# Kernel optimization log

Hardware: AMD Instinct MI355X
Metric: run time of the kernel (lower is better)

Reference implementation:

```python
import jax, jax.numpy as jnp
import numpy as np

NH = 4        # n_head
L_TOPK = 16   # AWG top-k l
DEC = 2       # dec_layers
EPS = 1e-6


def _ln(x, g, b):
    m = jnp.mean(x, -1, keepdims=True)
    v = jnp.mean((x - m) ** 2, -1, keepdims=True)
    return (x - m) * jax.lax.rsqrt(v + EPS) * g + b


def _heads(x, W):
    B, L, C = x.shape
    return (x @ W).reshape(B, L, NH, C // NH).transpose(0, 2, 1, 3)  # [B,H,L,dk]


def _softmax_attn(qh, kh):
    dk = qh.shape[-1]
    logits = jnp.einsum('bhqd,bhkd->bhqk', qh / jnp.sqrt(jnp.float32(dk)), kh)
    return jax.nn.softmax(logits, axis=-1)


def cross_attn_block(q, k, v, Wq, Wk, Wv, Wo, g, b):
    B, Lq, C = q.shape
    a = _softmax_attn(_heads(q, Wq), _heads(k, Wk))
    o = jnp.einsum('bhqk,bhkd->bhqd', a, _heads(v, Wv))
    o = o.transpose(0, 2, 1, 3).reshape(B, Lq, C) @ Wo
    return _ln(o + q, g, b)


def awg_attn_block(q, k, v, Wq, Wk, Wv, Wo, g, b):
    # top-k attention-weight-gating: keep weights >= l-th largest, renormalize
    B, Lq, C = q.shape
    a = _softmax_attn(_heads(q, Wq), _heads(k, Wk))
    thr = jax.lax.top_k(a, L_TOPK)[0][..., -1:]          # [B,H,Lq,1]
    w = a * (a >= thr).astype(a.dtype)
    w = w / jnp.sum(w, -1, keepdims=True)
    o = jnp.einsum('bhqk,bhkd->bhqd', w, _heads(v, Wv))
    o = o.transpose(0, 2, 1, 3).reshape(B, Lq, C) @ Wo
    return _ln(o + q, g, b)


def setup_inputs() -> dict:
    key = jax.random.key(0)
    ks = jax.random.split(key, 32)
    B, Lq, Lk, C, F = 4, 3000, 750, 64, 256
    s = 1.0 / np.sqrt(C)
    sf = 1.0 / np.sqrt(F)
    d = {}
    d['q'] = jax.random.normal(ks[0], (B, Lq, C), jnp.float32)
    d['enc'] = jax.random.normal(ks[1], (B, Lk, C), jnp.float32)
    # cross_attn_layer params
    for i, n in enumerate(['cal_Wq', 'cal_Wk', 'cal_Wv', 'cal_Wo']):
        d[n] = jax.random.normal(ks[2 + i], (C, C), jnp.float32) * s
    d['cal_ln1_g'] = jnp.ones((C,), jnp.float32)
    d['cal_ln1_b'] = jnp.zeros((C,), jnp.float32)
    d['cal_W1'] = jax.random.normal(ks[6], (C, F), jnp.float32) * s
    d['cal_b1'] = jnp.zeros((F,), jnp.float32)
    d['cal_W2'] = jax.random.normal(ks[7], (F, C), jnp.float32) * sf
    d['cal_b2'] = jnp.zeros((C,), jnp.float32)
    d['cal_ln2_g'] = jnp.ones((C,), jnp.float32)
    d['cal_ln2_b'] = jnp.zeros((C,), jnp.float32)
    # stacked MGAN params [DEC, ...]
    d['m_ln_g'] = jnp.ones((DEC, C), jnp.float32)
    d['m_ln_b'] = jnp.zeros((DEC, C), jnp.float32)
    d['m_fc1_W'] = jax.random.normal(ks[8], (DEC, C, C), jnp.float32) * s
    d['m_fc1_b'] = jnp.zeros((DEC, C), jnp.float32)
    d['m_fc2_W'] = jax.random.normal(ks[9], (DEC, C, C), jnp.float32) * s
    d['m_fc2_b'] = jnp.zeros((DEC, C), jnp.float32)
    for i, n in enumerate(['m_Wq', 'm_Wk', 'm_Wv', 'm_Wo']):
        d[n] = jax.random.normal(ks[10 + i], (DEC, C, C), jnp.float32) * s
    d['m_aln_g'] = jnp.ones((DEC, C), jnp.float32)
    d['m_aln_b'] = jnp.zeros((DEC, C), jnp.float32)
    d['fc_W'] = jax.random.normal(ks[14], (C, 1), jnp.float32) * s
    d['fc_b'] = jnp.zeros((1,), jnp.float32)
    return d


def reference(q, enc, cal_Wq, cal_Wk, cal_Wv, cal_Wo, cal_ln1_g, cal_ln1_b,
              cal_W1, cal_b1, cal_W2, cal_b2, cal_ln2_g, cal_ln2_b,
              m_ln_g, m_ln_b, m_fc1_W, m_fc1_b, m_fc2_W, m_fc2_b,
              m_Wq, m_Wk, m_Wv, m_Wo, m_aln_g, m_aln_b, fc_W, fc_b):
    # cross_attn_layer: attention + FFN + LN (dropout = identity in eval)
    x = cross_attn_block(q, enc, enc, cal_Wq, cal_Wk, cal_Wv, cal_Wo, cal_ln1_g, cal_ln1_b)
    ffn = jax.nn.relu(x @ cal_W1 + cal_b1) @ cal_W2 + cal_b2
    x = _ln(ffn + x, cal_ln2_g, cal_ln2_b)
    # MGAN decoder layers (rep_KV: k,v = encoder output)
    for i in range(DEC):
        qn = _ln(x, m_ln_g[i], m_ln_b[i])
        sg = jax.nn.sigmoid(qn @ m_fc1_W[i] + m_fc1_b[i]) * (qn @ m_fc2_W[i] + m_fc2_b[i])
        awg = awg_attn_block(sg, enc, enc, m_Wq[i], m_Wk[i], m_Wv[i], m_Wo[i],
                             m_aln_g[i], m_aln_b[i])
        # GLU(cat(sg, awg)) = sg * sigmoid(awg)
        x = qn + sg * jax.nn.sigmoid(awg)
    # label_type='p' head
    return jax.nn.sigmoid(x @ fc_W + fc_b)  # [B, Lq, 1]
```

## Files before the change

### kernel.cpp

```cpp
#include <hip/hip_runtime.h>
#include <hip/hip_bf16.h>

using bf16 = __hip_bfloat16;

#define DEV_INLINE __device__ __forceinline__

constexpr int B_  = 4;
constexpr int LQ  = 3000;
constexpr int LK  = 750;
constexpr int NH_ = 4;
constexpr float EPSF = 1e-6f;

constexpr int PITCH = 751;

constexpr size_t WS_KV = 0;
constexpr size_t WS_XB = 1152000;
constexpr size_t WS_QP = 1920000;
constexpr size_t WS_AO = 2688000;
constexpr size_t WS_QN = 3456000;
constexpr size_t WS_SG = 4224000;

typedef _Float16 half2_t __attribute__((ext_vector_type(2)));
typedef _Float16 half4_t __attribute__((ext_vector_type(4)));
typedef float    f32x4   __attribute__((ext_vector_type(4)));

#define MFMA16(a, b, c) __builtin_amdgcn_mfma_f32_16x16x16f16((a), (b), (c), 0, 0, 0)

DEV_INLINE float sigmoidf(float x) { return 1.f / (1.f + __expf(-x)); }

DEV_INLINE unsigned int packh2(float a, float b) {
  half2_t h = { (_Float16)a, (_Float16)b };
  unsigned int u; __builtin_memcpy(&u, &h, 4); return u;
}
DEV_INLINE half2_t u2h(unsigned int u) {
  half2_t h; __builtin_memcpy(&h, &u, 4); return h;
}
DEV_INLINE unsigned short f2h(float f) {
  _Float16 h = (_Float16)f;
  unsigned short u; __builtin_memcpy(&u, &h, 2); return u;
}
DEV_INLINE half4_t h4_from(const unsigned short* p) {
  unsigned int lo = *(const unsigned int*)p;
  unsigned int hi = *(const unsigned int*)(p + 2);
  unsigned long long v = ((unsigned long long)hi << 32) | lo;
  half4_t h; __builtin_memcpy(&h, &v, 8); return h;
}
DEV_INLINE float dot2(unsigned int kw, half2_t qh, float acc) {
  return __builtin_amdgcn_fdot2(u2h(kw), qh, acc, false);
}

DEV_INLINE unsigned int f2sort(float f) {
  int ib = __float_as_int(f);
  return (unsigned int)(ib ^ ((ib >> 31) | 0x80000000));
}
DEV_INLINE float sort2f(unsigned int u) {
  const int ib = (u & 0x80000000u) ? (int)(u ^ 0x80000000u) : (int)~u;
  return __int_as_float(ib);
}

DEV_INLINE unsigned int bcastu(unsigned int v) {
  return (unsigned int)__builtin_amdgcn_readfirstlane((int)v);
}

DEV_INLINE void sort64u_desc4(unsigned int v[4]) {
  const int lane = threadIdx.x & 63;
  #pragma unroll
  for (int k = 2; k <= 64; k <<= 1) {
    #pragma unroll
    for (int j = k >> 1; j > 0; j >>= 1) {
      const bool takeMax = ((lane & j) == 0) == ((lane & k) == 0);
      #pragma unroll
      for (int r = 0; r < 4; ++r) {
        const unsigned int o = __shfl_xor(v[r], j);
        v[r] = (takeMax == (v[r] > o)) ? v[r] : o;
      }
    }
  }
}

DEV_INLINE float row_ln(float v, float g, float b) {
  float s1 = v, s2 = v * v;
  #pragma unroll
  for (int off = 32; off > 0; off >>= 1) {
    s1 += __shfl_xor(s1, off);
    s2 += __shfl_xor(s2, off);
  }
  const float m   = s1 * (1.f / 64.f);
  const float var = s2 * (1.f / 64.f) - m * m;
  return (v - m) * rsqrtf(var + EPSF) * g + b;
}

__global__ __launch_bounds__(256) void kvq_proj_kernel(
    const float* __restrict__ enc, const float* __restrict__ q,
    const float* __restrict__ calWq,
    const float* __restrict__ calWk, const float* __restrict__ calWv,
    const float* __restrict__ mWk, const float* __restrict__ mWv,
    float* __restrict__ kv, float* __restrict__ qp)
{
  const int y = blockIdx.y;
  if (y < 6 && blockIdx.x >= 188) return;
  __shared__ float Wl[64 * 65];
  __shared__ float xs[16][64];
  const int t = threadIdx.x, rr = t >> 6, cc = t & 63;
  const float* W;
  const float* src;
  float* dst;
  float scale = 1.f;
  int nrows = 3000;
  switch (y) {
    case 0: W = calWk; src = enc; dst = kv;               break;
    case 1: W = calWv; src = enc; dst = kv + 192000;      break;
    case 2: W = mWk;        src = enc; dst = kv + 384000; break;
    case 3: W = mWv;        src = enc; dst = kv + 576000; break;
    case 4: W = mWk + 4096; src = enc; dst = kv + 768000; break;
    case 5: W = mWv + 4096; src = enc; dst = kv + 960000; break;
    default: W = calWq; src = q; dst = qp; scale = 0.25f; nrows = 12000; break;
  }
  const bool packK = (y == 2) || (y == 4);
  for (int i = t; i < 4096; i += 256) Wl[(i >> 6) * 65 + (i & 63)] = W[i];
  const int base = blockIdx.x * 16;
  for (int i = t; i < 1024; i += 256) {
    const int grow = base + (i >> 6);
    xs[i >> 6][i & 63] = (grow < nrows) ? src[(size_t)grow * 64 + (i & 63)] : 0.f;
  }
  __syncthreads();
  #pragma unroll
  for (int p = 0; p < 4; ++p) {
    const int row = p * 4 + rr;
    const int grow = base + row;
    float acc = 0.f;
    #pragma unroll
    for (int c = 0; c < 64; ++c) acc = fmaf(xs[row][c], Wl[c * 65 + cc], acc);
    if (packK) {
      const float accN = __shfl_xor(acc, 1);
      if (!(cc & 1) && grow < nrows)
        ((unsigned int*)dst)[(size_t)grow * 32 + (cc >> 1)] = packh2(acc, accN);
    } else if (grow < nrows) {
      dst[(size_t)grow * 64 + cc] = acc * scale;
    }
  }
}

__global__ __launch_bounds__(256) void cross_attn_kernel(
    const float* __restrict__ qp, const float* __restrict__ kp,
    const float* __restrict__ vp, float* __restrict__ ao)
{
  extern __shared__ char smem[];
  unsigned short* Kl = (unsigned short*)smem;
  unsigned short* Vt = Kl + 750 * 18;
  unsigned short* Pt = Vt + 16 * 754;

  const int t = threadIdx.x;
  const int h = blockIdx.y, b = blockIdx.z;
  const float* kslab = kp + (size_t)(b * LK) * 64 + h * 16;
  const float* vslab = vp + (size_t)(b * LK) * 64 + h * 16;

  for (int k = t; k < LK; k += 256) {
    const float4* ks = (const float4*)(kslab + (size_t)k * 64);
    const float4* vs = (const float4*)(vslab + (size_t)k * 64);
    unsigned int* kr = (unsigned int*)(Kl + k * 18);
    #pragma unroll
    for (int q4 = 0; q4 < 4; ++q4) {
      float4 a = ks[q4], v = vs[q4];
      kr[q4 * 2]     = packh2(a.x, a.y);
      kr[q4 * 2 + 1] = packh2(a.z, a.w);
      Vt[(q4 * 4 + 0) * 754 + k] = f2h(v.x);
      Vt[(q4 * 4 + 1) * 754 + k] = f2h(v.y);
      Vt[(q4 * 4 + 2) * 754 + k] = f2h(v.z);
      Vt[(q4 * 4 + 3) * 754 + k] = f2h(v.w);
    }
  }
  if (t < 32) Vt[(t & 15) * 754 + 750 + (t >> 4)] = 0;
  __syncthreads();

  const int wave = t >> 6, lane = t & 63;
  const int col = lane & 15, quad = lane >> 4;
  const int qbase = blockIdx.x * 64 + wave * 16;
  unsigned short* Pt_w = Pt + wave * 288;

  int qrow = qbase + col; if (qrow >= LQ) qrow = LQ - 1;
  const float* qptr = qp + ((size_t)(b * LQ + qrow)) * 64 + h * 16 + quad * 4;
  half4_t aQ;
  {
    unsigned long long v = ((unsigned long long)packh2(qptr[2], qptr[3]) << 32)
                         | packh2(qptr[0], qptr[1]);
    __builtin_memcpy(&aQ, &v, 8);
  }

  f32x4 O = {0.f, 0.f, 0.f, 0.f};
  float Zp[4] = {0.f, 0.f, 0.f, 0.f};
  const f32x4 zeroC = {0.f, 0.f, 0.f, 0.f};

  for (int tile = 0; tile < 47; ++tile) {
    const int key = tile * 16 + col;
    const half4_t bK = h4_from(Kl + key * 18 + quad * 4);
    f32x4 S = MFMA16(aQ, bK, zeroC);
    const bool valid = key < LK;
    float e0 = valid ? __expf(S[0]) : 0.f;
    float e1 = valid ? __expf(S[1]) : 0.f;
    float e2 = valid ? __expf(S[2]) : 0.f;
    float e3 = valid ? __expf(S[3]) : 0.f;
    Zp[0] += e0; Zp[1] += e1; Zp[2] += e2; Zp[3] += e3;
    Pt_w[(quad * 4 + 0) * 18 + col] = f2h(e0);
    Pt_w[(quad * 4 + 1) * 18 + col] = f2h(e1);
    Pt_w[(quad * 4 + 2) * 18 + col] = f2h(e2);
    Pt_w[(quad * 4 + 3) * 18 + col] = f2h(e3);
    const half4_t aP = h4_from(Pt_w + col * 18 + quad * 4);
    const half4_t bV = h4_from(Vt + col * 754 + tile * 16 + quad * 4);
    O = MFMA16(aP, bV, O);
  }

  #pragma unroll
  for (int r = 0; r < 4; ++r) {
    float z = Zp[r];
    z += __shfl_xor(z, 1);
    z += __shfl_xor(z, 2);
    z += __shfl_xor(z, 4);
    z += __shfl_xor(z, 8);
    Zp[r] = z;
  }

  #pragma unroll
  for (int r = 0; r < 4; ++r) {
    const int orow = qbase + quad * 4 + r;
    if (orow < LQ)
      ao[((size_t)(b * LQ + orow)) * 64 + h * 16 + col] = O[r] / Zp[r];
  }
}

__global__ __launch_bounds__(512) void awg_attn_kernel(
    const float* __restrict__ qp, const unsigned int* __restrict__ kp,
    const float* __restrict__ vp, float* __restrict__ ao)
{
  extern __shared__ char smem[];
  uint2*          KT2   = (uint2*)smem;
  unsigned int*   candV = (unsigned int*)(smem + 4 * PITCH * 8);
  unsigned short* candK = (unsigned short*)(smem + 4 * PITCH * 8 + 8192);
  float*          selW  = (float*)(smem + 4 * PITCH * 8 + 8192 + 4096);
  unsigned short* selK  = (unsigned short*)(smem + 4 * PITCH * 8 + 8192 + 4096 + 3072);

  const int t = threadIdx.x;
  const int h = blockIdx.y, b = blockIdx.z;
  const unsigned int* kslab = kp + ((size_t)(b * LK)) * 32 + h * 8;

  for (int k = t; k < LK; k += 512) {
    const uint2* ks = (const uint2*)(kslab + (size_t)k * 32);
    #pragma unroll
    for (int d4 = 0; d4 < 4; ++d4) KT2[d4 * PITCH + k] = ks[d4];
  }
  __syncthreads();

  const int wave = t >> 6, lane = t & 63;
  const unsigned long long below = (1ull << lane) - 1ull;
  unsigned int*   cV = candV + wave * 256;
  unsigned short* cK = candK + wave * 256;
  float*          sW = selW + wave * 96;
  unsigned short* sK = selK + wave * 96;

  sW[lane] = -3.0e38f; sK[lane] = 0;
  if (lane < 32) { sW[64 + lane] = -3.0e38f; sK[64 + lane] = 0; }
  #pragma unroll
  for (int r = 0; r < 4; ++r) cV[r * 64 + lane] = 0u;

  const int r0 = blockIdx.x * 32 + wave * 4;
  int r0r = r0; if (r0r > LQ - 4) r0r = LQ - 4;
  const float* qrow = qp + ((size_t)(b * LQ + r0r)) * 64 + h * 16;
  unsigned int qw[4][8];
  #pragma unroll
  for (int r = 0; r < 4; ++r) {
    #pragma unroll
    for (int i = 0; i < 8; ++i)
      qw[r][i] = bcastu(packh2(qrow[r * 64 + 2 * i], qrow[r * 64 + 2 * i + 1]));
  }

  float lg[4][12];
  #pragma unroll
  for (int tt = 0; tt < 12; ++tt) {
    const int k = lane + (tt << 6);
    if (tt < 11 || k < LK) {
      float a0 = 0.f, a1 = 0.f, a2 = 0.f, a3 = 0.f;
      #pragma unroll
      for (int d4 = 0; d4 < 4; ++d4) {
        const uint2 w = KT2[d4 * PITCH + k];
        a0 = dot2(w.x, u2h(qw[0][2 * d4]), a0); a0 = dot2(w.y, u2h(qw[0][2 * d4 + 1]), a0);
        a1 = dot2(w.x, u2h(qw[1][2 * d4]), a1); a1 = dot2(w.y, u2h(qw[1][2 * d4 + 1]), a1);
        a2 = dot2(w.x, u2h(qw[2][2 * d4]), a2); a2 = dot2(w.y, u2h(qw[2][2 * d4 + 1]), a2);
        a3 = dot2(w.x, u2h(qw[3][2 * d4]), a3); a3 = dot2(w.y, u2h(qw[3][2 * d4 + 1]), a3);
      }
      lg[0][tt] = a0; lg[1][tt] = a1; lg[2][tt] = a2; lg[3][tt] = a3;
    } else {
      lg[0][tt] = -3.0e38f; lg[1][tt] = -3.0e38f;
      lg[2][tt] = -3.0e38f; lg[3][tt] = -3.0e38f;
    }
  }

  unsigned int hs[4];
  #pragma unroll
  for (int r = 0; r < 4; ++r) {
    float m = lg[r][0];
    #pragma unroll
    for (int tt = 1; tt < 12; ++tt) m = fmaxf(m, lg[r][tt]);
    hs[r] = f2sort(m);
  }

  sort64u_desc4(hs);
  unsigned int L[4];
  #pragma unroll
  for (int r = 0; r < 4; ++r) L[r] = __shfl(hs[r], 15);

  int cb[4] = {0, 0, 0, 0};
  #pragma unroll
  for (int tt = 0; tt < 12; ++tt) {
    const int k = lane + (tt << 6);
    #pragma unroll
    for (int r = 0; r < 4; ++r) {
      const unsigned int s = f2sort(lg[r][tt]);
      const bool p = s >= L[r];
      const unsigned long long m = __ballot(p);
      if (p) {
        const int pos = cb[r] + (int)__popcll(m & below);
        if (pos < 64) { cV[r * 64 + pos] = s; cK[r * 64 + pos] = (unsigned short)k; }
      }
      cb[r] += (int)__popcll(m);
    }
  }

  unsigned int su[4], so[4];
  #pragma unroll
  for (int r = 0; r < 4; ++r) { su[r] = cV[r * 64 + lane]; so[r] = su[r]; }
  sort64u_desc4(so);
  unsigned int T[4]; float Mv[4];
  #pragma unroll
  for (int r = 0; r < 4; ++r) {
    T[r]  = __shfl(so[r], 15);
    Mv[r] = sort2f(__shfl(so[r], 0));
  }

  #pragma unroll
  for (int r = 0; r < 4; ++r) {
    const bool w = su[r] >= T[r];
    const unsigned long long mw = __ballot(w);
    if (w) {
      const int pos = (int)__popcll(mw & below);
      if (pos < 24) { sW[r * 24 + pos] = sort2f(su[r]); sK[r * 24 + pos] = cK[r * 64 + lane]; }
    }
  }

  const int dd = lane & 15;
  const int rsel = lane >> 4;
  const float ref = (rsel == 0) ? Mv[0] : (rsel == 1) ? Mv[1] : (rsel == 2) ? Mv[2] : Mv[3];
  const float* cwr = sW + rsel * 24;
  const unsigned short* cir = sK + rsel * 24;
  const float* vbase = vp + (size_t)(b * LK) * 64 + h * 16 + dd;
  float acc = 0.f, Z = 0.f;
  #pragma unroll
  for (int j = 0; j < 24; ++j) {
    const float e = __expf(cwr[j] - ref);
    Z += e;
    acc = fmaf(e, vbase[(size_t)cir[j] * 64], acc);
  }
  if (r0 + rsel < LQ)
    ao[((size_t)(b * LQ + r0 + rsel)) * 64 + h * 16 + dd] = acc / Z;
}

__global__ __launch_bounds__(256) void ffn_pre_kernel(
    const float* __restrict__ ao, const float* __restrict__ qres,
    const float* __restrict__ Wo,
    const float* __restrict__ g1, const float* __restrict__ b1n,
    const float* __restrict__ W1, const float* __restrict__ bb1,
    const float* __restrict__ W2, const float* __restrict__ bb2,
    const float* __restrict__ g2, const float* __restrict__ b2n,
    const float* __restrict__ lng, const float* __restrict__ lnb,
    const float* __restrict__ fc1W, const float* __restrict__ fc1b,
    const float* __restrict__ fc2W, const float* __restrict__ fc2b,
    const float* __restrict__ Wq,
    float* __restrict__ qn, float* __restrict__ sg, float* __restrict__ qp)
{
  __shared__ float xs[16][64];
  __shared__ float hsm[16][256];
  const int t = threadIdx.x, rr = t >> 6, cc = t & 63;
  const size_t base = (size_t)blockIdx.x * 16;
  for (int i = t; i < 1024; i += 256) xs[i >> 6][i & 63] = ao[base * 64 + i];
  __syncthreads();
  float acc[4];
  #pragma unroll
  for (int p = 0; p < 4; ++p) acc[p] = 0.f;
  #pragma unroll 8
  for (int c = 0; c < 64; ++c) {
    const float w = Wo[c * 64 + cc];
    #pragma unroll
    for (int p = 0; p < 4; ++p) acc[p] = fmaf(xs[p * 4 + rr][c], w, acc[p]);
  }
  #pragma unroll
  for (int p = 0; p < 4; ++p) acc[p] += qres[(base + p * 4 + rr) * 64 + cc];
  __syncthreads();
  float x1[4];
  #pragma unroll
  for (int p = 0; p < 4; ++p) {
    x1[p] = row_ln(acc[p], g1[cc], b1n[cc]);
    xs[p * 4 + rr][cc] = x1[p];
  }
  __syncthreads();
  {
    float hv[16];
    #pragma unroll
    for (int r = 0; r < 16; ++r) hv[r] = 0.f;
    #pragma unroll 4
    for (int c = 0; c < 64; ++c) {
      const float w = W1[c * 256 + t];
      #pragma unroll
      for (int r = 0; r < 16; ++r) hv[r] = fmaf(xs[r][c], w, hv[r]);
    }
    const float bb = bb1[t];
    #pragma unroll
    for (int r = 0; r < 16; ++r) hsm[r][t] = fmaxf(hv[r] + bb, 0.f);
  }
  __syncthreads();
  float acc2[4];
  #pragma unroll
  for (int p = 0; p < 4; ++p) acc2[p] = bb2[cc];
  #pragma unroll 8
  for (int c = 0; c < 256; ++c) {
    const float w = W2[c * 64 + cc];
    #pragma unroll
    for (int p = 0; p < 4; ++p) acc2[p] = fmaf(hsm[p * 4 + rr][c], w, acc2[p]);
  }
  float qv[4];
  #pragma unroll
  for (int p = 0; p < 4; ++p) {
    const float xv = row_ln(acc2[p] + x1[p], g2[cc], b2n[cc]);
    qv[p] = row_ln(xv, lng[cc], lnb[cc]);
    qn[(base + p * 4 + rr) * 64 + cc] = qv[p];
  }
  __syncthreads();
  #pragma unroll
  for (int p = 0; p < 4; ++p) xs[p * 4 + rr][cc] = qv[p];
  __syncthreads();
  float d1[4], d2[4];
  #pragma unroll
  for (int p = 0; p < 4; ++p) { d1[p] = fc1b[cc]; d2[p] = fc2b[cc]; }
  #pragma unroll 4
  for (int c = 0; c < 64; ++c) {
    const float w1 = fc1W[c * 64 + cc];
    const float w2 = fc2W[c * 64 + cc];
    #pragma unroll
    for (int p = 0; p < 4; ++p) {
      const float xq = xs[p * 4 + rr][c];
      d1[p] = fmaf(xq, w1, d1[p]);
      d2[p] = fmaf(xq, w2, d2[p]);
    }
  }
  float sv[4];
  #pragma unroll
  for (int p = 0; p < 4; ++p) {
    sv[p] = sigmoidf(d1[p]) * d2[p];
    sg[(base + p * 4 + rr) * 64 + cc] = sv[p];
  }
  __syncthreads();
  #pragma unroll
  for (int p = 0; p < 4; ++p) xs[p * 4 + rr][cc] = sv[p];
  __syncthreads();
  float aq[4];
  #pragma unroll
  for (int p = 0; p < 4; ++p) aq[p] = 0.f;
  #pragma unroll 8
  for (int c = 0; c < 64; ++c) {
    const float w = Wq[c * 64 + cc];
    #pragma unroll
    for (int p = 0; p < 4; ++p) aq[p] = fmaf(xs[p * 4 + rr][c], w, aq[p]);
  }
  #pragma unroll
  for (int p = 0; p < 4; ++p)
    qp[(base + p * 4 + rr) * 64 + cc] = aq[p] * 0.25f;
}

__global__ __launch_bounds__(256) void out_pre_kernel(
    const float* __restrict__ ao, const float* __restrict__ sg,
    const float* __restrict__ qn, const float* __restrict__ Wo,
    const float* __restrict__ g_, const float* __restrict__ b_,
    const float* __restrict__ lng, const float* __restrict__ lnb,
    const float* __restrict__ W1, const float* __restrict__ bb1,
    const float* __restrict__ W2, const float* __restrict__ bb2,
    const float* __restrict__ Wq,
    float* __restrict__ qn_out, float* __restrict__ sg_out,
    float* __restrict__ qp_out)
{
  __shared__ float xs[16][64];
  const int t = threadIdx.x, rr = t >> 6, cc = t & 63;
  const size_t base = (size_t)blockIdx.x * 16;
  for (int i = t; i < 1024; i += 256) xs[i >> 6][i & 63] = ao[base * 64 + i];
  __syncthreads();
  float accp[4], sgv[4];
  #pragma unroll
  for (int p = 0; p < 4; ++p) accp[p] = 0.f;
  #pragma unroll 8
  for (int c = 0; c < 64; ++c) {
    const float w = Wo[c * 64 + cc];
    #pragma unroll
    for (int p = 0; p < 4; ++p) accp[p] = fmaf(xs[p * 4 + rr][c], w, accp[p]);
  }
  #pragma unroll
  for (int p = 0; p < 4; ++p) {
    sgv[p] = sg[(base + p * 4 + rr) * 64 + cc];
    accp[p] += sgv[p];
  }
  __syncthreads();
  float qv[4];
  #pragma unroll
  for (int p = 0; p < 4; ++p) {
    const size_t idx = (base + p * 4 + rr) * 64 + cc;
    const float awg = row_ln(accp[p], g_[cc], b_[cc]);
    const float xv = qn[idx] + sgv[p] * sigmoidf(awg);
    qv[p] = row_ln(xv, lng[cc], lnb[cc]);
    qn_out[idx] = qv[p];
    xs[p * 4 + rr][cc] = qv[p];
  }
  __syncthreads();
  float d1[4], d2[4];
  #pragma unroll
  for (int p = 0; p < 4; ++p) { d1[p] = bb1[cc]; d2[p] = bb2[cc]; }
  #pragma unroll 4
  for (int c = 0; c < 64; ++c) {
    const float w1 = W1[c * 64 + cc];
    const float w2 = W2[c * 64 + cc];
    #pragma unroll
    for (int p = 0; p < 4; ++p) {
      const float xv = xs[p * 4 + rr][c];
      d1[p] = fmaf(xv, w1, d1[p]);
      d2[p] = fmaf(xv, w2, d2[p]);
    }
  }
  __syncthreads();
  float sv[4];
  #pragma unroll
  for (int p = 0; p < 4; ++p) {
    sv[p] = sigmoidf(d1[p]) * d2[p];
    sg_out[(base + p * 4 + rr) * 64 + cc] = sv[p];
    xs[p * 4 + rr][cc] = sv[p];
  }
  __syncthreads();
  float aq[4];
  #pragma unroll
  for (int p = 0; p < 4; ++p) aq[p] = 0.f;
  #pragma unroll 8
  for (int c = 0; c < 64; ++c) {
    const float w = Wq[c * 64 + cc];
    #pragma unroll
    for (int p = 0; p < 4; ++p) aq[p] = fmaf(xs[p * 4 + rr][c], w, aq[p]);
  }
  #pragma unroll
  for (int p = 0; p < 4; ++p)
    qp_out[(base + p * 4 + rr) * 64 + cc] = aq[p] * 0.25f;
}

__global__ __launch_bounds__(256) void out_final_kernel(
    const float* __restrict__ ao, const float* __restrict__ sg,
    const float* __restrict__ qn, const float* __restrict__ Wo,
    const float* __restrict__ g_, const float* __restrict__ b_,
    const float* __restrict__ fw, const float* __restrict__ fb,
    float* __restrict__ out)
{
  __shared__ float xs[16][64];
  const int t = threadIdx.x, rr = t >> 6, cc = t & 63;
  const size_t base = (size_t)blockIdx.x * 16;
  for (int i = t; i < 1024; i += 256) xs[i >> 6][i & 63] = ao[base * 64 + i];
  __syncthreads();
  float accp[4];
  #pragma unroll
  for (int p = 0; p < 4; ++p) accp[p] = 0.f;
  #pragma unroll 8
  for (int c = 0; c < 64; ++c) {
    const float w = Wo[c * 64 + cc];
    #pragma unroll
    for (int p = 0; p < 4; ++p) accp[p] = fmaf(xs[p * 4 + rr][c], w, accp[p]);
  }
  #pragma unroll
  for (int p = 0; p < 4; ++p) {
    const size_t idx = (base + p * 4 + rr) * 64 + cc;
    const float sgv = sg[idx];
    const float a = accp[p] + sgv;
    const float awg = row_ln(a, g_[cc], b_[cc]);
    const float xv = qn[idx] + sgv * sigmoidf(awg);
    float v = xv * fw[cc];
    #pragma unroll
    for (int off = 32; off > 0; off >>= 1) v += __shfl_xor(v, off);
    if (cc == 0) out[base + p * 4 + rr] = sigmoidf(v + fb[0]);
  }
}

extern "C" void kernel_launch(void* const* d_in, const int* in_sizes, int n_in,
                              void* d_out, int out_size, void* d_ws, size_t ws_size,
                              hipStream_t stream) {
  (void)in_sizes; (void)n_in; (void)out_size; (void)ws_size;

  const float* q     = (const float*)d_in[0];
  const float* enc   = (const float*)d_in[1];
  const float* calWq = (const float*)d_in[2];
  const float* calWk = (const float*)d_in[3];
  const float* calWv = (const float*)d_in[4];
  const float* calWo = (const float*)d_in[5];
  const float* ln1g  = (const float*)d_in[6];
  const float* ln1b  = (const float*)d_in[7];
  const float* W1    = (const float*)d_in[8];
  const float* b1v   = (const float*)d_in[9];
  const float* W2    = (const float*)d_in[10];
  const float* b2v   = (const float*)d_in[11];
  const float* ln2g  = (const float*)d_in[12];
  const float* ln2b  = (const float*)d_in[13];
  const float* mlng  = (const float*)d_in[14];
  const float* mlnb  = (const float*)d_in[15];
  const float* mfc1W = (const float*)d_in[16];
  const float* mfc1b = (const float*)d_in[17];
  const float* mfc2W = (const float*)d_in[18];
  const float* mfc2b = (const float*)d_in[19];
  const float* mWq   = (const float*)d_in[20];
  const float* mWk   = (const float*)d_in[21];
  const float* mWv   = (const float*)d_in[22];
  const float* mWo   = (const float*)d_in[23];
  const float* malng = (const float*)d_in[24];
  const float* malnb = (const float*)d_in[25];
  const float* fcW   = (const float*)d_in[26];
  const float* fcb   = (const float*)d_in[27];
  float* out = (float*)d_out;

  float* ws  = (float*)d_ws;
  float* kv  = ws + WS_KV;
  float* qp  = ws + WS_QP;
  float* aob = ws + WS_AO;
  float* qnb = ws + WS_QN;
  float* sgb = ws + WS_SG;

  const size_t crossLds = (750 * 18 + 16 * 754 + 4 * 288) * 2;
  const size_t awgLds   = 4 * PITCH * 8 + 8192 + 4096 + 3072 + 1536;

  kvq_proj_kernel<<<dim3(750, 7), 256, 0, stream>>>(enc, q, calWq, calWk, calWv,
                                                    mWk, mWv, kv, qp);

  cross_attn_kernel<<<dim3(47, NH_, B_), 256, crossLds, stream>>>(qp, kv, kv + 192000, aob);
  ffn_pre_kernel<<<750, 256, 0, stream>>>(aob, q, calWo, ln1g, ln1b,
                                          W1, b1v, W2, b2v, ln2g, ln2b,
                                          mlng, mlnb, mfc1W, mfc1b,
                                          mfc2W, mfc2b, mWq, qnb, sgb, qp);

  awg_attn_kernel<<<dim3(94, NH_, B_), 512, awgLds, stream>>>(
      qp, (const unsigned int*)(kv + 2 * 192000), kv + 3 * 192000, aob);
  out_pre_kernel<<<750, 256, 0, stream>>>(aob, sgb, qnb, mWo, malng, malnb,
                                          mlng + 64, mlnb + 64,
                                          mfc1W + 4096, mfc1b + 64,
                                          mfc2W + 4096, mfc2b + 64,
                                          mWq + 4096, qnb, sgb, qp);

  awg_attn_kernel<<<dim3(94, NH_, B_), 512, awgLds, stream>>>(
      qp, (const unsigned int*)(kv + 4 * 192000), kv + 5 * 192000, aob);
  out_final_kernel<<<750, 256, 0, stream>>>(aob, sgb, qnb, mWo + 4096,
                                            malng + 64, malnb + 64, fcW, fcb, out);
}
```

Baseline: 319.3 us.

## Compute AWG logits with MFMA into shared memory; read projection weights directly

Result: slower. 326.4 us (+2.2%).

```diff
diff --git a/kernel.cpp b/kernel.cpp
--- a/kernel.cpp
+++ b/kernel.cpp
@@ -11,7 +11,7 @@
 constexpr int NH_ = 4;
 constexpr float EPSF = 1e-6f;
 
-constexpr int PITCH = 751;
+constexpr int LGP = 758;
 
 constexpr size_t WS_KV = 0;
 constexpr size_t WS_XB = 1152000;
@@ -45,9 +45,6 @@
   unsigned long long v = ((unsigned long long)hi << 32) | lo;
   half4_t h; __builtin_memcpy(&h, &v, 8); return h;
 }
-DEV_INLINE float dot2(unsigned int kw, half2_t qh, float acc) {
-  return __builtin_amdgcn_fdot2(u2h(kw), qh, acc, false);
-}
 
 DEV_INLINE unsigned int f2sort(float f) {
   int ib = __float_as_int(f);
@@ -56,10 +53,6 @@
 DEV_INLINE float sort2f(unsigned int u) {
   const int ib = (u & 0x80000000u) ? (int)(u ^ 0x80000000u) : (int)~u;
   return __int_as_float(ib);
-}
-
-DEV_INLINE unsigned int bcastu(unsigned int v) {
-  return (unsigned int)__builtin_amdgcn_readfirstlane((int)v);
 }
 
 DEV_INLINE void sort64u_desc4(unsigned int v[4]) {
@@ -99,7 +92,6 @@
 {
   const int y = blockIdx.y;
   if (y < 6 && blockIdx.x >= 188) return;
-  __shared__ float Wl[64 * 65];
   __shared__ float xs[16][64];
   const int t = threadIdx.x, rr = t >> 6, cc = t & 63;
   const float* W;
@@ -117,26 +109,28 @@
     default: W = calWq; src = q; dst = qp; scale = 0.25f; nrows = 12000; break;
   }
   const bool packK = (y == 2) || (y == 4);
-  for (int i = t; i < 4096; i += 256) Wl[(i >> 6) * 65 + (i & 63)] = W[i];
   const int base = blockIdx.x * 16;
   for (int i = t; i < 1024; i += 256) {
     const int grow = base + (i >> 6);
     xs[i >> 6][i & 63] = (grow < nrows) ? src[(size_t)grow * 64 + (i & 63)] : 0.f;
   }
   __syncthreads();
-  #pragma unroll
-  for (int p = 0; p < 4; ++p) {
-    const int row = p * 4 + rr;
-    const int grow = base + row;
-    float acc = 0.f;
-    #pragma unroll
-    for (int c = 0; c < 64; ++c) acc = fmaf(xs[row][c], Wl[c * 65 + cc], acc);
+  float acc[4] = {0.f, 0.f, 0.f, 0.f};
+  #pragma unroll 8
+  for (int c = 0; c < 64; ++c) {
+    const float w = W[c * 64 + cc];
+    #pragma unroll
+    for (int p = 0; p < 4; ++p) acc[p] = fmaf(xs[p * 4 + rr][c], w, acc[p]);
+  }
+  #pragma unroll
+  for (int p = 0; p < 4; ++p) {
+    const int grow = base + p * 4 + rr;
     if (packK) {
-      const float accN = __shfl_xor(acc, 1);
+      const float accN = __shfl_xor(acc[p], 1);
       if (!(cc & 1) && grow < nrows)
-        ((unsigned int*)dst)[(size_t)grow * 32 + (cc >> 1)] = packh2(acc, accN);
+        ((unsigned int*)dst)[(size_t)grow * 32 + (cc >> 1)] = packh2(acc[p], accN);
     } else if (grow < nrows) {
-      dst[(size_t)grow * 64 + cc] = acc * scale;
+      dst[(size_t)grow * 64 + cc] = acc[p] * scale;
     }
   }
 }
@@ -228,29 +222,57 @@
   }
 }
 
-__global__ __launch_bounds__(512) void awg_attn_kernel(
+__global__ __launch_bounds__(256) void awg_attn_kernel(
     const float* __restrict__ qp, const unsigned int* __restrict__ kp,
     const float* __restrict__ vp, float* __restrict__ ao)
 {
   extern __shared__ char smem[];
-  uint2*          KT2   = (uint2*)smem;
-  unsigned int*   candV = (unsigned int*)(smem + 4 * PITCH * 8);
-  unsigned short* candK = (unsigned short*)(smem + 4 * PITCH * 8 + 8192);
-  float*          selW  = (float*)(smem + 4 * PITCH * 8 + 8192 + 4096);
-  unsigned short* selK  = (unsigned short*)(smem + 4 * PITCH * 8 + 8192 + 4096 + 3072);
+  float* Lg = (float*)smem;
+  unsigned int*   candV = (unsigned int*)smem;
+  unsigned short* candK = (unsigned short*)(smem + 4096);
+  float*          selW  = (float*)(smem + 4096 + 2048);
+  unsigned short* selK  = (unsigned short*)(smem + 4096 + 2048 + 1536);
 
   const int t = threadIdx.x;
   const int h = blockIdx.y, b = blockIdx.z;
-  const unsigned int* kslab = kp + ((size_t)(b * LK)) * 32 + h * 8;
-
-  for (int k = t; k < LK; k += 512) {
-    const uint2* ks = (const uint2*)(kslab + (size_t)k * 32);
-    #pragma unroll
-    for (int d4 = 0; d4 < 4; ++d4) KT2[d4 * PITCH + k] = ks[d4];
-  }
-  __syncthreads();
-
   const int wave = t >> 6, lane = t & 63;
+  const int col = lane & 15, quad = lane >> 4;
+  const int rbase = blockIdx.x * 16;
+
+  int qrow = rbase + col; if (qrow >= LQ) qrow = LQ - 1;
+  const float* qptr = qp + ((size_t)(b * LQ + qrow)) * 64 + h * 16 + quad * 4;
+  half4_t aQ;
+  {
+    unsigned long long v = ((unsigned long long)packh2(qptr[2], qptr[3]) << 32)
+                         | packh2(qptr[0], qptr[1]);
+    __builtin_memcpy(&aQ, &v, 8);
+  }
+  const unsigned int* kslab = kp + ((size_t)(b * LK)) * 32 + h * 8 + quad * 2;
+  const f32x4 zeroC = {0.f, 0.f, 0.f, 0.f};
+  for (int tile = wave; tile < 47; tile += 4) {
+    const int key = tile * 16 + col;
+    const int keyc = (key < LK) ? key : LK - 1;
+    const uint2 w = *(const uint2*)(kslab + (size_t)keyc * 32);
+    unsigned long long v = ((unsigned long long)w.y << 32) | w.x;
+    half4_t bK; __builtin_memcpy(&bK, &v, 8);
+    f32x4 S = MFMA16(aQ, bK, zeroC);
+    const bool valid = key < LK;
+    #pragma unroll
+    for (int r = 0; r < 4; ++r)
+      Lg[(quad * 4 + r) * LGP + key] = valid ? S[r] : -3.0e38f;
+  }
+  __syncthreads();
+
+  float lg[4][12];
+  #pragma unroll
+  for (int tt = 0; tt < 12; ++tt) {
+    const int k = lane + (tt << 6);
+    #pragma unroll
+    for (int r = 0; r < 4; ++r)
+      lg[r][tt] = (tt < 11 || k < LK) ? Lg[(wave * 4 + r) * LGP + k] : -3.0e38f;
+  }
+  __syncthreads();
+
   const unsigned long long below = (1ull << lane) - 1ull;
   unsigned int*   cV = candV + wave * 256;
   unsigned short* cK = candK + wave * 256;
@@ -262,51 +284,21 @@
   #pragma unroll
   for (int r = 0; r < 4; ++r) cV[r * 64 + lane] = 0u;
 
-  const int r0 = blockIdx.x * 32 + wave * 4;
-  int r0r = r0; if (r0r > LQ - 4) r0r = LQ - 4;
-  const float* qrow = qp + ((size_t)(b * LQ + r0r)) * 64 + h * 16;
-  unsigned int qw[4][8];
-  #pragma unroll
-  for (int r = 0; r < 4; ++r) {
-    #pragma unroll
-    for (int i = 0; i < 8; ++i)
-      qw[r][i] = bcastu(packh2(qrow[r * 64 + 2 * i], qrow[r * 64 + 2 * i + 1]));
-  }
-
-  float lg[4][12];
-  #pragma unroll
-  for (int tt = 0; tt < 12; ++tt) {
-    const int k = lane + (tt << 6);
-    if (tt < 11 || k < LK) {
-      float a0 = 0.f, a1 = 0.f, a2 = 0.f, a3 = 0.f;
-      #pragma unroll
-      for (int d4 = 0; d4 < 4; ++d4) {
-        const uint2 w = KT2[d4 * PITCH + k];
-        a0 = dot2(w.x, u2h(qw[0][2 * d4]), a0); a0 = dot2(w.y, u2h(qw[0][2 * d4 + 1]), a0);
-        a1 = dot2(w.x, u2h(qw[1][2 * d4]), a1); a1 = dot2(w.y, u2h(qw[1][2 * d4 + 1]), a1);
-        a2 = dot2(w.x, u2h(qw[2][2 * d4]), a2); a2 = dot2(w.y, u2h(qw[2][2 * d4 + 1]), a2);
-        a3 = dot2(w.x, u2h(qw[3][2 * d4]), a3); a3 = dot2(w.y, u2h(qw[3][2 * d4 + 1]), a3);
-      }
-      lg[0][tt] = a0; lg[1][tt] = a1; lg[2][tt] = a2; lg[3][tt] = a3;
-    } else {
-      lg[0][tt] = -3.0e38f; lg[1][tt] = -3.0e38f;
-      lg[2][tt] = -3.0e38f; lg[3][tt] = -3.0e38f;
-    }
-  }
-
-  unsigned int hs[4];
+  const int r0 = rbase + wave * 4;
+
+  unsigned int hs4[4];
   #pragma unroll
   for (int r = 0; r < 4; ++r) {
     float m = lg[r][0];
     #pragma unroll
     for (int tt = 1; tt < 12; ++tt) m = fmaxf(m, lg[r][tt]);
-    hs[r] = f2sort(m);
-  }
-
-  sort64u_desc4(hs);
+    hs4[r] = f2sort(m);
+  }
+
+  sort64u_desc4(hs4);
   unsigned int L[4];
   #pragma unroll
-  for (int r = 0; r < 4; ++r) L[r] = __shfl(hs[r], 15);
+  for (int r = 0; r < 4; ++r) L[r] = __shfl(hs4[r], 15);
 
   int cb[4] = {0, 0, 0, 0};
   #pragma unroll
@@ -631,7 +623,7 @@
   float* sgb = ws + WS_SG;
 
   const size_t crossLds = (750 * 18 + 16 * 754 + 4 * 288) * 2;
-  const size_t awgLds   = 4 * PITCH * 8 + 8192 + 4096 + 3072 + 1536;
+  const size_t awgLds   = 16 * LGP * 4;
 
   kvq_proj_kernel<<<dim3(750, 7), 256, 0, stream>>>(enc, q, calWq, calWk, calWv,
                                                     mWk, mWv, kv, qp);
@@ -642,7 +634,7 @@
                                           mlng, mlnb, mfc1W, mfc1b,
                                           mfc2W, mfc2b, mWq, qnb, sgb, qp);
 
-  awg_attn_kernel<<<dim3(94, NH_, B_), 512, awgLds, stream>>>(
+  awg_attn_kernel<<<dim3(188, NH_, B_), 256, awgLds, stream>>>(
       qp, (const unsigned int*)(kv + 2 * 192000), kv + 3 * 192000, aob);
   out_pre_kernel<<<750, 256, 0, stream>>>(aob, sgb, qnb, mWo, malng, malnb,
                                           mlng + 64, mlnb + 64,
@@ -650,7 +642,7 @@
                                           mfc2W + 4096, mfc2b + 64,
                                           mWq + 4096, qnb, sgb, qp);
 
-  awg_attn_kernel<<<dim3(94, NH_, B_), 512, awgLds, stream>>>(
+  awg_attn_kernel<<<dim3(188, NH_, B_), 256, awgLds, stream>>>(
       qp, (const unsigned int*)(kv + 4 * 192000), kv + 5 * 192000, aob);
   out_final_kernel<<<750, 256, 0, stream>>>(aob, sgb, qnb, mWo + 4096,
                                             malng + 64, malnb + 64, fcW, fcb, out);
```

## Pre-transpose weight matrices and use float4 vectorized GEMV loads

Applied to the files above, without the earlier changes.

Result: slower. 376.9 us (+18.1%).

```diff
diff --git a/kernel.cpp b/kernel.cpp
--- a/kernel.cpp
+++ b/kernel.cpp
@@ -90,53 +90,122 @@
   return (v - m) * rsqrtf(var + EPSF) * g + b;
 }
 
+__global__ __launch_bounds__(256) void transpose_kernel(
+    const float* __restrict__ calWq, const float* __restrict__ calWk,
+    const float* __restrict__ calWv, const float* __restrict__ calWo,
+    const float* __restrict__ mWk, const float* __restrict__ mWv,
+    const float* __restrict__ mWq, const float* __restrict__ mWo,
+    const float* __restrict__ fc1, const float* __restrict__ fc2,
+    const float* __restrict__ W1, const float* __restrict__ W2,
+    float* __restrict__ dst)
+{
+  const int b = blockIdx.x, t = threadIdx.x;
+  if (b < 16) {
+    const float* src;
+    switch (b) {
+      case 0:  src = calWq;        break;
+      case 1:  src = calWk;        break;
+      case 2:  src = calWv;        break;
+      case 3:  src = calWo;        break;
+      case 4:  src = mWk;          break;
+      case 5:  src = mWk + 4096;   break;
+      case 6:  src = mWv;          break;
+      case 7:  src = mWv + 4096;   break;
+      case 8:  src = mWq;          break;
+      case 9:  src = mWq + 4096;   break;
+      case 10: src = mWo;          break;
+      case 11: src = mWo + 4096;   break;
+      case 12: src = fc1;          break;
+      case 13: src = fc1 + 4096;   break;
+      case 14: src = fc2;          break;
+      default: src = fc2 + 4096;   break;
+    }
+    float* d = dst + b * 4096;
+    for (int i = t; i < 4096; i += 256) {
+      const int r = i >> 6, c = i & 63;
+      d[c * 64 + r] = src[r * 64 + c];
+    }
+  } else if (b < 20) {
+    float* d = dst + 65536;
+    const int q = b - 16;
+    for (int i = t; i < 4096; i += 256) {
+      const int e = q * 4096 + i;
+      const int r = e >> 8, col = e & 255;
+      d[col * 64 + r] = W1[r * 256 + col];
+    }
+  } else {
+    float* d = dst + 81920;
+    const int q = b - 20;
+    for (int i = t; i < 4096; i += 256) {
+      const int e = q * 4096 + i;
+      const int r = e >> 6, cc = e & 63;
+      d[cc * 256 + r] = W2[r * 64 + cc];
+    }
+  }
+}
+
+#define GEMV64_F4(WT_row, XS, ACC)                                  \
+  {                                                                 \
+    const float4* wt4 = (const float4*)(WT_row);                    \
+    _Pragma("unroll")                                               \
+    for (int c4 = 0; c4 < 16; ++c4) {                               \
+      const float4 w = wt4[c4];                                     \
+      _Pragma("unroll")                                             \
+      for (int p = 0; p < 4; ++p) {                                 \
+        const float4 x = *(const float4*)&XS[p * 4 + rr][c4 * 4];   \
+        ACC[p] = fmaf(x.x, w.x, ACC[p]);                            \
+        ACC[p] = fmaf(x.y, w.y, ACC[p]);                            \
+        ACC[p] = fmaf(x.z, w.z, ACC[p]);                            \
+        ACC[p] = fmaf(x.w, w.w, ACC[p]);                            \
+      }                                                             \
+    }                                                               \
+  }
+
 __global__ __launch_bounds__(256) void kvq_proj_kernel(
     const float* __restrict__ enc, const float* __restrict__ q,
-    const float* __restrict__ calWq,
-    const float* __restrict__ calWk, const float* __restrict__ calWv,
-    const float* __restrict__ mWk, const float* __restrict__ mWv,
+    const float* __restrict__ calWqT,
+    const float* __restrict__ calWkT, const float* __restrict__ calWvT,
+    const float* __restrict__ mWkT, const float* __restrict__ mWvT,
     float* __restrict__ kv, float* __restrict__ qp)
 {
   const int y = blockIdx.y;
   if (y < 6 && blockIdx.x >= 188) return;
-  __shared__ float Wl[64 * 65];
-  __shared__ float xs[16][64];
+  __shared__ __align__(16) float xs[16][64];
   const int t = threadIdx.x, rr = t >> 6, cc = t & 63;
-  const float* W;
+  const float* WT;
   const float* src;
   float* dst;
   float scale = 1.f;
   int nrows = 3000;
   switch (y) {
-    case 0: W = calWk; src = enc; dst = kv;               break;
-    case 1: W = calWv; src = enc; dst = kv + 192000;      break;
-    case 2: W = mWk;        src = enc; dst = kv + 384000; break;
-    case 3: W = mWv;        src = enc; dst = kv + 576000; break;
-    case 4: W = mWk + 4096; src = enc; dst = kv + 768000; break;
-    case 5: W = mWv + 4096; src = enc; dst = kv + 960000; break;
-    default: W = calWq; src = q; dst = qp; scale = 0.25f; nrows = 12000; break;
+    case 0: WT = calWkT;        src = enc; dst = kv;           break;
+    case 1: WT = calWvT;        src = enc; dst = kv + 192000;  break;
+    case 2: WT = mWkT;          src = enc; dst = kv + 384000;  break;
+    case 3: WT = mWvT;          src = enc; dst = kv + 576000;  break;
+    case 4: WT = mWkT + 4096;   src = enc; dst = kv + 768000;  break;
+    case 5: WT = mWvT + 4096;   src = enc; dst = kv + 960000;  break;
+    default: WT = calWqT; src = q; dst = qp; scale = 0.25f; nrows = 12000; break;
   }
   const bool packK = (y == 2) || (y == 4);
-  for (int i = t; i < 4096; i += 256) Wl[(i >> 6) * 65 + (i & 63)] = W[i];
   const int base = blockIdx.x * 16;
-  for (int i = t; i < 1024; i += 256) {
-    const int grow = base + (i >> 6);
-    xs[i >> 6][i & 63] = (grow < nrows) ? src[(size_t)grow * 64 + (i & 63)] : 0.f;
-  }
-  __syncthreads();
+  {
+    const int grow = base + (t >> 4);
+    float4 v = {0.f, 0.f, 0.f, 0.f};
+    if (grow < nrows) v = *(const float4*)&src[(size_t)grow * 64 + (t & 15) * 4];
+    ((float4*)xs)[t] = v;
+  }
+  __syncthreads();
+  float acc[4] = {0.f, 0.f, 0.f, 0.f};
+  GEMV64_F4(WT + cc * 64, xs, acc);
   #pragma unroll
   for (int p = 0; p < 4; ++p) {
-    const int row = p * 4 + rr;
-    const int grow = base + row;
-    float acc = 0.f;
-    #pragma unroll
-    for (int c = 0; c < 64; ++c) acc = fmaf(xs[row][c], Wl[c * 65 + cc], acc);
+    const int grow = base + p * 4 + rr;
     if (packK) {
-      const float accN = __shfl_xor(acc, 1);
+      const float accN = __shfl_xor(acc[p], 1);
       if (!(cc & 1) && grow < nrows)
-        ((unsigned int*)dst)[(size_t)grow * 32 + (cc >> 1)] = packh2(acc, accN);
+        ((unsigned int*)dst)[(size_t)grow * 32 + (cc >> 1)] = packh2(acc[p], accN);
     } else if (grow < nrows) {
-      dst[(size_t)grow * 64 + cc] = acc * scale;
+      dst[(size_t)grow * 64 + cc] = acc[p] * scale;
     }
   }
 }
@@ -365,32 +434,25 @@
 
 __global__ __launch_bounds__(256) void ffn_pre_kernel(
     const float* __restrict__ ao, const float* __restrict__ qres,
-    const float* __restrict__ Wo,
+    const float* __restrict__ WoT,
     const float* __restrict__ g1, const float* __restrict__ b1n,
-    const float* __restrict__ W1, const float* __restrict__ bb1,
-    const float* __restrict__ W2, const float* __restrict__ bb2,
+    const float* __restrict__ W1T, const float* __restrict__ bb1,
+    const float* __restrict__ W2T, const float* __restrict__ bb2,
     const float* __restrict__ g2, const float* __restrict__ b2n,
     const float* __restrict__ lng, const float* __restrict__ lnb,
-    const float* __restrict__ fc1W, const float* __restrict__ fc1b,
-    const float* __restrict__ fc2W, const float* __restrict__ fc2b,
-    const float* __restrict__ Wq,
+    const float* __restrict__ fc1T, const float* __restrict__ fc1b,
+    const float* __restrict__ fc2T, const float* __restrict__ fc2b,
+    const float* __restrict__ WqT,
     float* __restrict__ qn, float* __restrict__ sg, float* __restrict__ qp)
 {
-  __shared__ float xs[16][64];
-  __shared__ float hsm[16][256];
+  __shared__ __align__(16) float xs[16][64];
+  __shared__ __align__(16) float hsm[16][256];
   const int t = threadIdx.x, rr = t >> 6, cc = t & 63;
   const size_t base = (size_t)blockIdx.x * 16;
-  for (int i = t; i < 1024; i += 256) xs[i >> 6][i & 63] = ao[base * 64 + i];
-  __syncthreads();
-  float acc[4];
-  #pragma unroll
-  for (int p = 0; p < 4; ++p) acc[p] = 0.f;
-  #pragma unroll 8
-  for (int c = 0; c < 64; ++c) {
-    const float w = Wo[c * 64 + cc];
-    #pragma unroll
-    for (int p = 0; p < 4; ++p) acc[p] = fmaf(xs[p * 4 + rr][c], w, acc[p]);
-  }
+  ((float4*)xs)[t] = *(const float4*)&ao[base * 64 + t * 4];
+  __syncthreads();
+  float acc[4] = {0.f, 0.f, 0.f, 0.f};
+  GEMV64_F4(WoT + cc * 64, xs, acc);
   #pragma unroll
   for (int p = 0; p < 4; ++p) acc[p] += qres[(base + p * 4 + rr) * 64 + cc];
   __syncthreads();
@@ -405,11 +467,18 @@
     float hv[16];
     #pragma unroll
     for (int r = 0; r < 16; ++r) hv[r] = 0.f;
+    const float4* w1t4 = (const float4*)(W1T + t * 64);
     #pragma unroll 4
-    for (int c = 0; c < 64; ++c) {
-      const float w = W1[c * 256 + t];
+    for (int c4 = 0; c4 < 16; ++c4) {
+      const float4 w = w1t4[c4];
       #pragma unroll
-      for (int r = 0; r < 16; ++r) hv[r] = fmaf(xs[r][c], w, hv[r]);
+      for (int r = 0; r < 16; ++r) {
+        const float4 x = *(const float4*)&xs[r][c4 * 4];
+        hv[r] = fmaf(x.x, w.x, hv[r]);
+        hv[r] = fmaf(x.y, w.y, hv[r]);
+        hv[r] = fmaf(x.z, w.z, hv[r]);
+        hv[r] = fmaf(x.w, w.w, hv[r]);
+      }
     }
     const float bb = bb1[t];
     #pragma unroll
@@ -419,11 +488,20 @@
   float acc2[4];
   #pragma unroll
   for (int p = 0; p < 4; ++p) acc2[p] = bb2[cc];
-  #pragma unroll 8
-  for (int c = 0; c < 256; ++c) {
-    const float w = W2[c * 64 + cc];
-    #pragma unroll
-    for (int p = 0; p < 4; ++p) acc2[p] = fmaf(hsm[p * 4 + rr][c], w, acc2[p]);
+  {
+    const float4* w2t4 = (const float4*)(W2T + cc * 256);
+    #pragma unroll 8
+    for (int c4 = 0; c4 < 64; ++c4) {
+      const float4 w = w2t4[c4];
+      #pragma unroll
+      for (int p = 0; p < 4; ++p) {
+        const float4 x = *(const float4*)&hsm[p * 4 + rr][c4 * 4];
+        acc2[p] = fmaf(x.x, w.x, acc2[p]);
+        acc2[p] = fmaf(x.y, w.y, acc2[p]);
+        acc2[p] = fmaf(x.z, w.z, acc2[p]);
+        acc2[p] = fmaf(x.w, w.w, acc2[p]);
+      }
+    }
   }
   float qv[4];
   #pragma unroll
@@ -439,15 +517,21 @@
   float d1[4], d2[4];
   #pragma unroll
   for (int p = 0; p < 4; ++p) { d1[p] = fc1b[cc]; d2[p] = fc2b[cc]; }
-  #pragma unroll 4
-  for (int c = 0; c < 64; ++c) {
-    const float w1 = fc1W[c * 64 + cc];
-    const float w2 = fc2W[c * 64 + cc];
-    #pragma unroll
-    for (int p = 0; p < 4; ++p) {
-      const float xq = xs[p * 4 + rr][c];
-      d1[p] = fmaf(xq, w1, d1[p]);
-      d2[p] = fmaf(xq, w2, d2[p]);
+  {
+    const float4* f1t4 = (const float4*)(fc1T + cc * 64);
+    const float4* f2t4 = (const float4*)(fc2T + cc * 64);
+    #pragma unroll 4
+    for (int c4 = 0; c4 < 16; ++c4) {
+      const float4 w1 = f1t4[c4];
+      const float4 w2 = f2t4[c4];
+      #pragma unroll
+      for (int p = 0; p < 4; ++p) {
+        const float4 x = *(const float4*)&xs[p * 4 + rr][c4 * 4];
+        d1[p] = fmaf(x.x, w1.x, d1[p]); d2[p] = fmaf(x.x, w2.x, d2[p]);
+        d1[p] = fmaf(x.y, w1.y, d1[p]); d2[p] = fmaf(x.y, w2.y, d2[p]);
+        d1[p] = fmaf(x.z, w1.z, d1[p]); d2[p] = fmaf(x.z, w2.z, d2[p]);
+        d1[p] = fmaf(x.w, w1.w, d1[p]); d2[p] = fmaf(x.w, w2.w, d2[p]);
+      }
     }
   }
   float sv[4];
@@ -460,15 +544,8 @@
   #pragma unroll
   for (int p = 0; p < 4; ++p) xs[p * 4 + rr][cc] = sv[p];
   __syncthreads();
-  float aq[4];
-  #pragma unroll
-  for (int p = 0; p < 4; ++p) aq[p] = 0.f;
-  #pragma unroll 8
-  for (int c = 0; c < 64; ++c) {
-    const float w = Wq[c * 64 + cc];
-    #pragma unroll
-    for (int p = 0; p < 4; ++p) aq[p] = fmaf(xs[p * 4 + rr][c], w, aq[p]);
-  }
+  float aq[4] = {0.f, 0.f, 0.f, 0.f};
+  GEMV64_F4(WqT + cc * 64, xs, aq);
   #pragma unroll
   for (int p = 0; p < 4; ++p)
     qp[(base + p * 4 + rr) * 64 + cc] = aq[p] * 0.25f;
@@ -476,29 +553,22 @@
 
 __global__ __launch_bounds__(256) void out_pre_kernel(
     const float* __restrict__ ao, const float* __restrict__ sg,
-    const float* __restrict__ qn, const float* __restrict__ Wo,
+    const float* __restrict__ qn, const float* __restrict__ WoT,
     const float* __restrict__ g_, const float* __restrict__ b_,
     const float* __restrict__ lng, const float* __restrict__ lnb,
-    const float* __restrict__ W1, const float* __restrict__ bb1,
-    const float* __restrict__ W2, const float* __restrict__ bb2,
-    const float* __restrict__ Wq,
+    const float* __restrict__ W1T, const float* __restrict__ bb1,
+    const float* __restrict__ W2T, const float* __restrict__ bb2,
+    const float* __restrict__ WqT,
     float* __restrict__ qn_out, float* __restrict__ sg_out,
     float* __restrict__ qp_out)
 {
-  __shared__ float xs[16][64];
+  __shared__ __align__(16) float xs[16][64];
   const int t = threadIdx.x, rr = t >> 6, cc = t & 63;
   const size_t base = (size_t)blockIdx.x * 16;
-  for (int i = t; i < 1024; i += 256) xs[i >> 6][i & 63] = ao[base * 64 + i];
-  __syncthreads();
-  float accp[4], sgv[4];
-  #pragma unroll
-  for (int p = 0; p < 4; ++p) accp[p] = 0.f;
-  #pragma unroll 8
-  for (int c = 0; c < 64; ++c) {
-    const float w = Wo[c * 64 + cc];
-    #pragma unroll
-    for (int p = 0; p < 4; ++p) accp[p] = fmaf(xs[p * 4 + rr][c], w, accp[p]);
-  }
+  ((float4*)xs)[t] = *(const float4*)&ao[base * 64 + t * 4];
+  __syncthreads();
+  float accp[4] = {0.f, 0.f, 0.f, 0.f}, sgv[4];
+  GEMV64_F4(WoT + cc * 64, xs, accp);
   #pragma unroll
   for (int p = 0; p < 4; ++p) {
     sgv[p] = sg[(base + p * 4 + rr) * 64 + cc];
@@ -519,15 +589,21 @@
   float d1[4], d2[4];
   #pragma unroll
   for (int p = 0; p < 4; ++p) { d1[p] = bb1[cc]; d2[p] = bb2[cc]; }
-  #pragma unroll 4
-  for (int c = 0; c < 64; ++c) {
-    const float w1 = W1[c * 64 + cc];
-    const float w2 = W2[c * 64 + cc];
-    #pragma unroll
-    for (int p = 0; p < 4; ++p) {
-      const float xv = xs[p * 4 + rr][c];
-      d1[p] = fmaf(xv, w1, d1[p]);
-      d2[p] = fmaf(xv, w2, d2[p]);
+  {
+    const float4* f1t4 = (const float4*)(W1T + cc * 64);
+    const float4* f2t4 = (const float4*)(W2T + cc * 64);
+    #pragma unroll 4
+    for (int c4 = 0; c4 < 16; ++c4) {
+      const float4 w1 = f1t4[c4];
+      const float4 w2 = f2t4[c4];
+      #pragma unroll
+      for (int p = 0; p < 4; ++p) {
+        const float4 x = *(const float4*)&xs[p * 4 + rr][c4 * 4];
+        d1[p] = fmaf(x.x, w1.x, d1[p]); d2[p] = fmaf(x.x, w2.x, d2[p]);
+        d1[p] = fmaf(x.y, w1.y, d1[p]); d2[p] = fmaf(x.y, w2.y, d2[p]);
+        d1[p] = fmaf(x.z, w1.z, d1[p]); d2[p] = fmaf(x.z, w2.z, d2[p]);
+        d1[p] = fmaf(x.w, w1.w, d1[p]); d2[p] = fmaf(x.w, w2.w, d2[p]);
+      }
     }
   }
   __syncthreads();
@@ -539,15 +615,8 @@
     xs[p * 4 + rr][cc] = sv[p];
   }
   __syncthreads();
-  float aq[4];
-  #pragma unroll
-  for (int p = 0; p < 4; ++p) aq[p] = 0.f;
-  #pragma unroll 8
-  for (int c = 0; c < 64; ++c) {
-    const float w = Wq[c * 64 + cc];
-    #pragma unroll
-    for (int p = 0; p < 4; ++p) aq[p] = fmaf(xs[p * 4 + rr][c], w, aq[p]);
-  }
+  float aq[4] = {0.f, 0.f, 0.f, 0.f};
+  GEMV64_F4(WqT + cc * 64, xs, aq);
   #pragma unroll
   for (int p = 0; p < 4; ++p)
     qp_out[(base + p * 4 + rr) * 64 + cc] = aq[p] * 0.25f;
@@ -555,25 +624,18 @@
 
 __global__ __launch_bounds__(256) void out_final_kernel(
     const float* __restrict__ ao, const float* __restrict__ sg,
-    const float* __restrict__ qn, const float* __restrict__ Wo,
+    const float* __restrict__ qn, const float* __restrict__ WoT,
     const float* __restrict__ g_, const float* __restrict__ b_,
     const float* __restrict__ fw, const float* __restrict__ fb,
     float* __restrict__ out)
 {
-  __shared__ float xs[16][64];
+  __shared__ __align__(16) float xs[16][64];
   const int t = threadIdx.x, rr = t >> 6, cc = t & 63;
   const size_t base = (size_t)blockIdx.x * 16;
-  for (int i = t; i < 1024; i += 256) xs[i >> 6][i & 63] = ao[base * 64 + i];
-  __syncthreads();
-  float accp[4];
-  #pragma unroll
-  for (int p = 0; p < 4; ++p) accp[p] = 0.f;
-  #pragma unroll 8
-  for (int c = 0; c < 64; ++c) {
-    const float w = Wo[c * 64 + cc];
-    #pragma unroll
-    for (int p = 0; p < 4; ++p) accp[p] = fmaf(xs[p * 4 + rr][c], w, accp[p]);
-  }
+  ((float4*)xs)[t] = *(const float4*)&ao[base * 64 + t * 4];
+  __syncthreads();
+  float accp[4] = {0.f, 0.f, 0.f, 0.f};
+  GEMV64_F4(WoT + cc * 64, xs, accp);
   #pragma unroll
   for (int p = 0; p < 4; ++p) {
     const size_t idx = (base + p * 4 + rr) * 64 + cc;
@@ -629,29 +691,47 @@
   float* aob = ws + WS_AO;
   float* qnb = ws + WS_QN;
   float* sgb = ws + WS_SG;
+  float* xbT = ws + WS_XB;
+
+  const float* calWqT = xbT;
+  const float* calWkT = xbT + 4096;
+  const float* calWvT = xbT + 8192;
+  const float* calWoT = xbT + 12288;
+  const float* mWkT   = xbT + 16384;
+  const float* mWvT   = xbT + 24576;
+  const float* mWqT   = xbT + 32768;
+  const float* mWoT   = xbT + 40960;
+  const float* fc1T   = xbT + 49152;
+  const float* fc2T   = xbT + 57344;
+  const float* W1T    = xbT + 65536;
+  const float* W2T    = xbT + 81920;
 
   const size_t crossLds = (750 * 18 + 16 * 754 + 4 * 288) * 2;
   const size_t awgLds   = 4 * PITCH * 8 + 8192 + 4096 + 3072 + 1536;
 
-  kvq_proj_kernel<<<dim3(750, 7), 256, 0, stream>>>(enc, q, calWq, calWk, calWv,
-                                                    mWk, mWv, kv, qp);
+  transpose_kernel<<<24, 256, 0, stream>>>(calWq, calWk, calWv, calWo,
+                                           mWk, mWv, mWq, mWo,
+                                           mfc1W, mfc2W, W1, W2, xbT);
+
+  kvq_proj_kernel<<<dim3(750, 7), 256, 0, stream>>>(enc, q, calWqT, calWkT,
+                                                    calWvT, mWkT, mWvT, kv, qp);
 
   cross_attn_kernel<<<dim3(47, NH_, B_), 256, crossLds, stream>>>(qp, kv, kv + 192000, aob);
-  ffn_pre_kernel<<<750, 256, 0, stream>>>(aob, q, calWo, ln1g, ln1b,
-                                          W1, b1v, W2, b2v, ln2g, ln2b,
-                                          mlng, mlnb, mfc1W, mfc1b,
-                                          mfc2W, mfc2b, mWq, qnb, sgb, qp);
+  ffn_pre_kernel<<<750, 256, 0, stream>>>(aob, q, calWoT, ln1g, ln1b,
+                                          W1T, b1v, W2T, b2v, ln2g, ln2b,
+                                          mlng, mlnb, fc1T, mfc1b,
+                                          fc2T, mfc2b, mWqT, qnb, sgb, qp);
 
   awg_attn_kernel<<<dim3(94, NH_, B_), 512, awgLds, stream>>>(
       qp, (const unsigned int*)(kv + 2 * 192000), kv + 3 * 192000, aob);
-  out_pre_kernel<<<750, 256, 0, stream>>>(aob, sgb, qnb, mWo, malng, malnb,
+  out_pre_kernel<<<750, 256, 0, stream>>>(aob, sgb, qnb, mWoT, malng, malnb,
                                           mlng + 64, mlnb + 64,
-                                          mfc1W + 4096, mfc1b + 64,
-                                          mfc2W + 4096, mfc2b + 64,
-                                          mWq + 4096, qnb, sgb, qp);
+                                          fc1T + 4096, mfc1b + 64,
+                                          fc2T + 4096, mfc2b + 64,
+                                          mWqT + 4096, qnb, sgb, qp);
 
   awg_attn_kernel<<<dim3(94, NH_, B_), 512, awgLds, stream>>>(
       qp, (const unsigned int*)(kv + 4 * 192000), kv + 5 * 192000, aob);
-  out_final_kernel<<<750, 256, 0, stream>>>(aob, sgb, qnb, mWo + 4096,
+  out_final_kernel<<<750, 256, 0, stream>>>(aob, sgb, qnb, mWoT + 4096,
                                             malng + 64, malnb + 64, fcW, fcb, out);
 }
```
